# Kernel tuning notes

Measured on AMD Instinct MI355X. Metric: run time of the kernel, lower is better.

Reference implementation:

```python
import jax, jax.numpy as jnp
import numpy as np

N, E = 3000, 48000
IN_C, HID, OUT_C = 16, 64, 16
K1 = (N + 1) // 2          # ceil(0.5*N) = 1500
K2 = (K1 + 1) // 2         # ceil(0.5*K1) = 750


def _glorot(k, fi, fo):
    return jax.random.normal(k, (fi, fo), jnp.float32) / jnp.sqrt(jnp.float32(fi))


def setup_inputs() -> dict:
    key = jax.random.key(0)
    ks = jax.random.split(key, 10)
    x = jax.random.normal(ks[0], (N, IN_C), jnp.float32)
    edge_index = jax.random.randint(ks[1], (2, E), 0, N, dtype=jnp.int32)
    return {
        "x": x,
        "edge_index": edge_index,
        "W0": _glorot(ks[2], IN_C, HID), "b0": jnp.zeros((HID,), jnp.float32),
        "W1": _glorot(ks[3], HID, HID), "b1": jnp.zeros((HID,), jnp.float32),
        "W2": _glorot(ks[4], HID, HID), "b2": jnp.zeros((HID,), jnp.float32),
        "p1": jax.random.normal(ks[5], (HID,), jnp.float32),
        "p2": jax.random.normal(ks[6], (HID,), jnp.float32),
        "Wu0": _glorot(ks[7], HID, HID), "bu0": jnp.zeros((HID,), jnp.float32),
        "Wu1": _glorot(ks[8], HID, OUT_C), "bu1": jnp.zeros((OUT_C,), jnp.float32),
    }


def _gcn(h, A, W, b):
    # GCNConv(improved=True): add self-loops with weight 2, symmetric gcn_norm
    # with degree taken over the target (column) axis; aggregate at targets.
    n = A.shape[0]
    eye = jnp.eye(n, dtype=A.dtype)
    Ah = A + 2.0 * eye
    deg = Ah.sum(axis=0)                      # in-degree (PyG gcn_norm uses col)
    dinv = jnp.where(deg > 0, jax.lax.rsqrt(deg), 0.0)
    M = dinv[:, None] * Ah * dinv[None, :]    # M[s, t] = norm of edge s->t
    return M.T @ (h @ W) + b                  # out[t] = sum_s M[s,t] * h[s] W


def _augment(A):
    # augment_adj: remove self loops, add self loops (w=1), A <- A @ A, drop diag
    n = A.shape[0]
    eye = jnp.eye(n, dtype=A.dtype)
    A1 = A * (1.0 - eye) + eye
    A2 = A1 @ A1
    return A2 * (1.0 - eye)


def _topk_pool(h, A, p, k):
    # TopKPooling defaults: score = tanh((x . p) / ||p||), multiplier = 1
    score = jnp.tanh((h @ p) / jnp.linalg.norm(p))
    _, perm = jax.lax.top_k(score, k)
    hp = h[perm] * score[perm][:, None]
    Ap = A[perm][:, perm]
    return hp, Ap, perm


def _graph_unet(x, A0, W0, b0, W1, b1, W2, b2, p1, p2, Wu0, bu0, Wu1, bu1):
    act = jnp.tanh
    x = act(_gcn(x, A0, W0, b0))
    res0 = x
    # down level 1
    xp, A1, perm1 = _topk_pool(x, _augment(A0), p1, K1)
    x = act(_gcn(xp, A1, W1, b1))
    res1 = x
    # down level 2 (deepest; not stored as residual)
    xp, A2, perm2 = _topk_pool(x, _augment(A1), p2, K2)
    x = act(_gcn(xp, A2, W2, b2))
    # up to level 1 (sum_res=True)
    up = jnp.zeros_like(res1).at[perm2].set(x)
    x = act(_gcn(res1 + up, A1, Wu0, bu0))
    # up to level 0 (last up conv: no activation)
    up = jnp.zeros_like(res0).at[perm1].set(x)
    return _gcn(res0 + up, A0, Wu1, bu1)


def reference(x, edge_index, W0, b0, W1, b1, W2, b2, p1, p2, Wu0, bu0, Wu1, bu1):
    # dense adjacency from COO edge list with unit edge weights (duplicates sum)
    A0 = jnp.zeros((N, N), jnp.float32).at[edge_index[0], edge_index[1]].add(1.0)
    # eval-mode forward of PUnetStepV2: drift = GraphUNet(x, edge_index)
    return _graph_unet(x, A0, W0, b0, W1, b1, W2, b2, p1, p2, Wu0, bu0, Wu1, bu1)
```

## Files before the change

### kernel.cpp

```cpp
#include <hip/hip_runtime.h>

#define NN   3000
#define EE   48000
#define KK1  1500
#define KK2  750
#define KK2P 752
#define HIDC 64
#define SLOT 64

#define CAP0  64
#define CAP1  768
#define CAP2  768
#define CAPB0 64
#define CAPMAX 768


__global__ void k_zero_i32(int* __restrict__ p, int n) {
    int i = blockIdx.x * blockDim.x + threadIdx.x;
    if (i < n) p[i] = 0;
}

__global__ void k_edge_slots(const int* __restrict__ ei, int* __restrict__ cntraw,
                             int* __restrict__ slots) {
    int e = blockIdx.x * blockDim.x + threadIdx.x;
    if (e >= EE) return;
    int s = ei[e];
    int t = ei[EE + e];
    int idx = atomicAdd(&cntraw[t], 1);
    if (idx < SLOT) slots[t * SLOT + idx] = s;
}

__global__ void k_csr0_sort(const int* __restrict__ cntraw, const int* __restrict__ slots,
                            int* __restrict__ cols, float* __restrict__ vals,
                            int* __restrict__ cnt, float* __restrict__ dinv) {
    int row = blockIdx.x * (blockDim.x >> 6) + (threadIdx.x >> 6);
    int lane = threadIdx.x & 63;
    int raw = cntraw[row];
    int nz = raw < SLOT ? raw : SLOT;
    int my = (lane < nz) ? slots[row * SLOT + lane] : 0x7FFFFFFF;
    int dup_before = 0, equal_total = 0;
    for (int f = 0; f < 64; ++f) {
        int cf = __shfl(my, f, 64);
        if (cf == my) { equal_total++; if (f < lane) dup_before++; }
    }
    bool leader = (lane < nz) && (dup_before == 0);
    unsigned long long lm = __ballot(leader);
    int dl = 0;
    unsigned long long m = lm;
    while (m) {
        int f = __builtin_ctzll(m); m &= m - 1;
        int cf = __shfl(my, f, 64);
        dl += (cf < my);
    }
    if (leader) {
        cols[(size_t)row * CAP0 + dl] = my;
        vals[(size_t)row * CAP0 + dl] = (float)equal_total;
    }
    if (lane == 0) {
        cnt[row] = __popcll(lm);
        dinv[row] = rsqrtf((float)raw + 2.0f);
    }
}

__global__ void k_xw_scale(const float* __restrict__ h, const float* __restrict__ up,
                           const int* __restrict__ selpos,
                           const float* __restrict__ W, const float* __restrict__ dinv,
                           float* __restrict__ g, int n, int IC, int OC) {
    int row = blockIdx.x;
    int c = threadIdx.x;
    __shared__ float hr[64];
    if (c < IC) {
        float v = h[(size_t)row * IC + c];
        if (selpos) {
            int sp = selpos[row];
            if (sp >= 0) v += up[(size_t)sp * IC + c];
        }
        hr[c] = v;
    }
    __syncthreads();
    if (c >= OC) return;
    float acc = 0.0f;
    for (int k = 0; k < IC; ++k) acc += hr[k] * W[k * OC + c];
    g[(size_t)row * OC + c] = dinv[row] * acc;
}

__global__ void k_gcn_agg_csr(const int* __restrict__ cols, const float* __restrict__ vals,
                              const int* __restrict__ cnt, int CAP,
                              const float* __restrict__ g, const float* __restrict__ dinv,
                              const float* __restrict__ bias, float* __restrict__ out,
                              int n, int C, int do_tanh,
                              const float* __restrict__ p, float* __restrict__ score) {
    int row = blockIdx.x;
    int w = threadIdx.x >> 6;
    int lane = threadIdx.x & 63;
    int nz = cnt[row];
    const int*   rc = cols + (size_t)row * CAP;
    const float* rv = vals + (size_t)row * CAP;
    bool act = lane < C;
    float a0 = 0.f, a1 = 0.f, a2 = 0.f, a3 = 0.f;
    float a4 = 0.f, a5 = 0.f, a6 = 0.f, a7 = 0.f;
    for (int e = 8 * w; e + 8 <= nz; e += 32) {
        int   c0 = rc[e],     c1 = rc[e + 1], c2 = rc[e + 2], c3 = rc[e + 3];
        int   c4 = rc[e + 4], c5 = rc[e + 5], c6 = rc[e + 6], c7 = rc[e + 7];
        float v0 = rv[e],     v1 = rv[e + 1], v2 = rv[e + 2], v3 = rv[e + 3];
        float v4 = rv[e + 4], v5 = rv[e + 5], v6 = rv[e + 6], v7 = rv[e + 7];
        if (act) {
            a0 += v0 * g[(size_t)c0 * C + lane];
            a1 += v1 * g[(size_t)c1 * C + lane];
            a2 += v2 * g[(size_t)c2 * C + lane];
            a3 += v3 * g[(size_t)c3 * C + lane];
            a4 += v4 * g[(size_t)c4 * C + lane];
            a5 += v5 * g[(size_t)c5 * C + lane];
            a6 += v6 * g[(size_t)c6 * C + lane];
            a7 += v7 * g[(size_t)c7 * C + lane];
        }
    }
    if (w == 0) {
        for (int e = nz & ~7; e < nz; ++e)
            if (act) a0 += rv[e] * g[(size_t)rc[e] * C + lane];
    }
    __shared__ float red[4][64];
    red[w][lane] = ((a0 + a1) + (a2 + a3)) + ((a4 + a5) + (a6 + a7));
    __syncthreads();
    if (w == 0) {
        float o = 0.f;
        if (act) {
            float a = (red[0][lane] + red[1][lane]) + (red[2][lane] + red[3][lane])
                    + 2.0f * g[(size_t)row * C + lane];
            o = dinv[row] * a + bias[lane];
            if (do_tanh) o = tanhf(o);
            out[(size_t)row * C + lane] = o;
        }
        if (p) {
            float pv = p[lane];
            float d = o * pv, pp = pv * pv;
            for (int off = 32; off; off >>= 1) {
                d  += __shfl_down(d, off, 64);
                pp += __shfl_down(pp, off, 64);
            }
            if (lane == 0) score[row] = tanhf(d * rsqrtf(pp));
        }
    }
}

__global__ void k_topk(const float* __restrict__ score, const float* __restrict__ h,
                       int n, int k, int* __restrict__ perm, int* __restrict__ selpos,
                       float* __restrict__ hp) {
    int i = blockIdx.x;
    float si = score[i];
    int r = 0;
    for (int j = threadIdx.x; j < n; j += blockDim.x) {
        float sj = score[j];
        r += (sj > si) || (sj == si && j < i);
    }
    int lane = threadIdx.x & 63, wid = threadIdx.x >> 6;
    for (int off = 32; off; off >>= 1) r += __shfl_down(r, off, 64);
    __shared__ int red[4];
    __shared__ int srank;
    if (lane == 0) red[wid] = r;
    __syncthreads();
    if (threadIdx.x == 0) {
        int rank = red[0] + red[1] + red[2] + red[3];
        srank = rank;
        selpos[i] = (rank < k) ? rank : -1;
        if (rank < k) perm[rank] = i;
    }
    __syncthreads();
    int rank = srank;
    if (rank < k && threadIdx.x < HIDC)
        hp[(size_t)rank * HIDC + threadIdx.x] = h[(size_t)i * HIDC + threadIdx.x] * si;
}

__global__ void k_bcolcsr(const int* __restrict__ cols, const float* __restrict__ vals,
                          const int* __restrict__ cnt, int CAPS,
                          const int* __restrict__ selpos, int n,
                          int* __restrict__ bcC, float* __restrict__ bcV,
                          int* __restrict__ bcN, int CAPB) {
    int row = blockIdx.x * (blockDim.x >> 6) + (threadIdx.x >> 6);
    int lane = threadIdx.x & 63;
    if (row >= n) return;
    int nz = cnt[row];
    int base = 0;
    for (int e0 = 0; e0 < nz; e0 += 64) {
        int e = e0 + lane;
        int j = -1; float v = 0.0f;
        if (e < nz) {
            int c = cols[(size_t)row * CAPS + e];
            if (c != row) { j = selpos[c]; v = vals[(size_t)row * CAPS + e]; }
        }
        unsigned long long mb = __ballot(j >= 0);
        if (j >= 0) {
            int idx = base + __popcll(mb & ((1ull << lane) - 1ull));
            if (idx < CAPB) { bcC[(size_t)row * CAPB + idx] = j; bcV[(size_t)row * CAPB + idx] = v; }
        }
        base += __popcll(mb);
    }
    if (lane == 0) {
        int jd = selpos[row];
        if (jd >= 0 && base < CAPB) {
            bcC[(size_t)row * CAPB + base] = jd;
            bcV[(size_t)row * CAPB + base] = 1.0f;
            base++;
        }
        bcN[row] = base < CAPB ? base : CAPB;
    }
}

__global__ void k_aug_sparse(const int* __restrict__ perm,
                             const int* __restrict__ colsS, const float* __restrict__ valsS,
                             const int* __restrict__ cntS, int CAPS,
                             const int* __restrict__ bcC, const float* __restrict__ bcV,
                             const int* __restrict__ bcN, int CAPB, int kk,
                             int* __restrict__ colsD, float* __restrict__ valsD,
                             int* __restrict__ cntD, float* __restrict__ dinvD, int CAPD) {
    __shared__ float srow[1504];
    __shared__ float ssum[4];
    int i = blockIdx.x;
    int pi = perm[i];
    int nzS = cntS[pi];
    for (int t = threadIdx.x; t < 1504; t += blockDim.x) srow[t] = 0.0f;
    __syncthreads();
    int w = threadIdx.x >> 6, lane = threadIdx.x & 63;
    for (int ee = w; ee <= nzS; ee += 4) {
        int k; float kv;
        if (ee == nzS) { k = pi; kv = 1.0f; }
        else {
            k = colsS[(size_t)pi * CAPS + ee];
            if (k == pi) continue;
            kv = valsS[(size_t)pi * CAPS + ee];
        }
        int bn = bcN[k];
        const int*   bc = bcC + (size_t)k * CAPB;
        const float* bv = bcV + (size_t)k * CAPB;
        for (int t = lane; t < bn; t += 64)
            atomicAdd(&srow[bc[t]], kv * bv[t]);
    }
    __syncthreads();
    if (threadIdx.x == 0) srow[i] = 0.0f;
    __syncthreads();
    float psum = 0.0f;
    for (int t = threadIdx.x; t < kk; t += blockDim.x) psum += srow[t];
    for (int off = 32; off; off >>= 1) psum += __shfl_down(psum, off, 64);
    if (lane == 0) ssum[w] = psum;
    __syncthreads();
    if (w == 0) {
        if (lane == 0)
            dinvD[i] = rsqrtf((ssum[0] + ssum[1]) + (ssum[2] + ssum[3]) + 2.0f);
        int base = 0;
        for (int c0 = 0; c0 < kk; c0 += 64) {
            int c = c0 + lane;
            float v = (c < kk) ? srow[c] : 0.0f;
            unsigned long long mb = __ballot(v != 0.0f);
            if (v != 0.0f) {
                int idx = base + __popcll(mb & ((1ull << lane) - 1ull));
                if (idx < CAPD) {
                    colsD[(size_t)i * CAPD + idx] = c;
                    valsD[(size_t)i * CAPD + idx] = v;
                }
            }
            base += __popcll(mb);
        }
        if (lane == 0) cntD[i] = base < CAPD ? base : CAPD;
    }
}

__global__ void k_bcol_scatter(const int* __restrict__ cols, const float* __restrict__ vals,
                               const int* __restrict__ cnt, int CAP,
                               const int* __restrict__ selpos, float* __restrict__ Bcol, int ldb) {
    int row = blockIdx.x;
    float4* rowp = (float4*)(Bcol + (size_t)row * ldb);
    float4 z = {0.f, 0.f, 0.f, 0.f};
    for (int q = threadIdx.x; q < (ldb >> 2); q += blockDim.x) rowp[q] = z;
    __syncthreads();
    int nz = cnt[row];
    for (int e = threadIdx.x; e < nz; e += blockDim.x) {
        int c = cols[(size_t)row * CAP + e];
        if (c == row) continue;
        int j = selpos[c];
        if (j >= 0) Bcol[(size_t)row * ldb + j] = vals[(size_t)row * CAP + e];
    }
    if (threadIdx.x == 0) {
        int j = selpos[row];
        if (j >= 0) Bcol[(size_t)row * ldb + j] = 1.0f;
    }
}

__global__ void k_aug_fused(const int* __restrict__ perm,
                            const int* __restrict__ colsS, const float* __restrict__ valsS,
                            const int* __restrict__ cntS, int CAPS,
                            const float* __restrict__ Bcol, int ldb, int kk,
                            int* __restrict__ colsD, float* __restrict__ valsD,
                            int* __restrict__ cntD, float* __restrict__ dinvD, int CAPD) {
    __shared__ int   scol[CAPMAX];
    __shared__ float sval[CAPMAX];
    __shared__ float srow[1504];
    __shared__ float ssum[4];
    int i = blockIdx.x;
    int pi = perm[i];
    int nz = cntS[pi];
    for (int e = threadIdx.x; e < nz; e += blockDim.x) {
        int c = colsS[(size_t)pi * CAPS + e];
        scol[e] = c;
        sval[e] = (c == pi) ? 0.0f : valsS[(size_t)pi * CAPS + e];
    }
    __syncthreads();
    float psum = 0.0f;
    for (int j0 = threadIdx.x * 4; j0 < kk; j0 += blockDim.x * 4) {
        int j4 = j0 >> 2;
        float4 a = ((const float4*)(Bcol + (size_t)pi * ldb))[j4];
        float4 acc1 = {0.f, 0.f, 0.f, 0.f};
        int e = 0;
        for (; e + 8 <= nz; e += 8) {
            float v0 = sval[e],     v1 = sval[e + 1], v2 = sval[e + 2], v3 = sval[e + 3];
            float v4 = sval[e + 4], v5 = sval[e + 5], v6 = sval[e + 6], v7 = sval[e + 7];
            float4 b0 = ((const float4*)(Bcol + (size_t)scol[e]     * ldb))[j4];
            float4 b1 = ((const float4*)(Bcol + (size_t)scol[e + 1] * ldb))[j4];
            float4 b2 = ((const float4*)(Bcol + (size_t)scol[e + 2] * ldb))[j4];
            float4 b3 = ((const float4*)(Bcol + (size_t)scol[e + 3] * ldb))[j4];
            float4 b4 = ((const float4*)(Bcol + (size_t)scol[e + 4] * ldb))[j4];
            float4 b5 = ((const float4*)(Bcol + (size_t)scol[e + 5] * ldb))[j4];
            float4 b6 = ((const float4*)(Bcol + (size_t)scol[e + 6] * ldb))[j4];
            float4 b7 = ((const float4*)(Bcol + (size_t)scol[e + 7] * ldb))[j4];
            a.x += v0 * b0.x + v1 * b1.x + v2 * b2.x + v3 * b3.x;
            a.y += v0 * b0.y + v1 * b1.y + v2 * b2.y + v3 * b3.y;
            a.z += v0 * b0.z + v1 * b1.z + v2 * b2.z + v3 * b3.z;
            a.w += v0 * b0.w + v1 * b1.w + v2 * b2.w + v3 * b3.w;
            acc1.x += v4 * b4.x + v5 * b5.x + v6 * b6.x + v7 * b7.x;
            acc1.y += v4 * b4.y + v5 * b5.y + v6 * b6.y + v7 * b7.y;
            acc1.z += v4 * b4.z + v5 * b5.z + v6 * b6.z + v7 * b7.z;
            acc1.w += v4 * b4.w + v5 * b5.w + v6 * b6.w + v7 * b7.w;
        }
        for (; e < nz; ++e) {
            float v = sval[e];
            float4 b = ((const float4*)(Bcol + (size_t)scol[e] * ldb))[j4];
            a.x += v * b.x; a.y += v * b.y; a.z += v * b.z; a.w += v * b.w;
        }
        a.x += acc1.x; a.y += acc1.y; a.z += acc1.z; a.w += acc1.w;
        if (i >= j0 && i < j0 + 4) ((float*)&a)[i - j0] = 0.0f;
        *(float4*)(srow + j0) = a;
        psum += (a.x + a.y) + (a.z + a.w);
    }
    int lane = threadIdx.x & 63, w = threadIdx.x >> 6;
    for (int off = 32; off; off >>= 1) psum += __shfl_down(psum, off, 64);
    if (lane == 0) ssum[w] = psum;
    __syncthreads();
    if (w == 0) {
        if (lane == 0)
            dinvD[i] = rsqrtf((ssum[0] + ssum[1]) + (ssum[2] + ssum[3]) + 2.0f);
        int base = 0;
        for (int c0 = 0; c0 < kk; c0 += 64) {
            int c = c0 + lane;
            float v = (c < kk) ? srow[c] : 0.0f;
            unsigned long long mb = __ballot(v != 0.0f);
            if (v != 0.0f) {
                int idx = base + __popcll(mb & ((1ull << lane) - 1ull));
                if (idx < CAPD) {
                    colsD[(size_t)i * CAPD + idx] = c;
                    valsD[(size_t)i * CAPD + idx] = v;
                }
            }
            base += __popcll(mb);
        }
        if (lane == 0) cntD[i] = base < CAPD ? base : CAPD;
    }
}


extern "C" void kernel_launch(void* const* d_in, const int* in_sizes, int n_in,
                              void* d_out, int out_size, void* d_ws, size_t ws_size,
                              hipStream_t stream) {
    const float* x   = (const float*)d_in[0];
    const int*   ei  = (const int*)d_in[1];
    const float* W0  = (const float*)d_in[2];
    const float* b0  = (const float*)d_in[3];
    const float* W1  = (const float*)d_in[4];
    const float* b1  = (const float*)d_in[5];
    const float* W2  = (const float*)d_in[6];
    const float* b2  = (const float*)d_in[7];
    const float* p1  = (const float*)d_in[8];
    const float* p2  = (const float*)d_in[9];
    const float* Wu0 = (const float*)d_in[10];
    const float* bu0 = (const float*)d_in[11];
    const float* Wu1 = (const float*)d_in[12];
    const float* bu1 = (const float*)d_in[13];
    float* out = (float*)d_out;

    float* fw = (float*)d_ws;
    size_t off = 0;
    int*   slots  = (int*)(fw + off); off += (size_t)NN * SLOT;
    int*   cntraw = (int*)(fw + off); off += NN;
    int*   cols0  = (int*)(fw + off); off += (size_t)NN * CAP0;
    float* vals0  = fw + off;         off += (size_t)NN * CAP0;
    int*   cols1  = (int*)(fw + off); off += (size_t)KK1 * CAP1;
    float* vals1  = fw + off;         off += (size_t)KK1 * CAP1;
    int*   cols2  = (int*)(fw + off); off += (size_t)KK2 * CAP2;
    float* vals2  = fw + off;         off += (size_t)KK2 * CAP2;
    int*   bc0C   = (int*)(fw + off); off += (size_t)NN * CAPB0;
    float* bc0V   = fw + off;         off += (size_t)NN * CAPB0;
    int*   bc0N   = (int*)(fw + off); off += NN;
    float* Bcol2  = fw + off;         off += (size_t)KK1 * KK2P;
    int*   cnt0   = (int*)(fw + off); off += NN;
    int*   cnt1   = (int*)(fw + off); off += KK1;
    int*   cnt2   = (int*)(fw + off); off += KK2 + 2;
    float* g      = fw + off; off += (size_t)NN * HIDC;
    float* res0   = fw + off; off += (size_t)NN * HIDC;
    float* res1   = fw + off; off += (size_t)KK1 * HIDC;
    float* hp     = fw + off; off += (size_t)KK1 * HIDC;
    float* hp2    = fw + off; off += (size_t)KK2 * HIDC;
    float* x2     = fw + off; off += (size_t)KK2 * HIDC;
    float* xu     = fw + off; off += (size_t)KK1 * HIDC;
    float* sc1    = fw + off; off += NN;
    float* sc2    = fw + off; off += KK1;
    float* dinv0  = fw + off; off += NN;
    float* dinv1  = fw + off; off += KK1;
    float* dinv2  = fw + off; off += KK2 + 2;
    int* perm1    = (int*)(fw + off); off += KK1;
    int* perm2    = (int*)(fw + off); off += KK2 + 2;
    int* selpos1  = (int*)(fw + off); off += NN;
    int* selpos2  = (int*)(fw + off); off += KK1;
    if (ws_size < off * sizeof(float)) return;

    dim3 b64(64), b256(256);

    k_zero_i32<<<dim3((NN + 255) / 256), b256, 0, stream>>>(cntraw, NN);
    k_edge_slots<<<dim3((EE + 255) / 256), b256, 0, stream>>>(ei, cntraw, slots);
    k_csr0_sort<<<dim3(NN / 4), b256, 0, stream>>>(cntraw, slots, cols0, vals0, cnt0, dinv0);

    k_xw_scale<<<dim3(NN), b64, 0, stream>>>(x, nullptr, nullptr, W0, dinv0, g, NN, 16, 64);
    k_gcn_agg_csr<<<dim3(NN), b256, 0, stream>>>(cols0, vals0, cnt0, CAP0, g, dinv0, b0, res0, NN, 64, 1, p1, sc1);

    k_topk<<<dim3(NN), b256, 0, stream>>>(sc1, res0, NN, KK1, perm1, selpos1, hp);
    k_bcolcsr<<<dim3(NN / 4), b256, 0, stream>>>(cols0, vals0, cnt0, CAP0, selpos1, NN, bc0C, bc0V, bc0N, CAPB0);
    k_aug_sparse<<<dim3(KK1), b256, 0, stream>>>(perm1, cols0, vals0, cnt0, CAP0,
                                                 bc0C, bc0V, bc0N, CAPB0, KK1,
                                                 cols1, vals1, cnt1, dinv1, CAP1);

    k_xw_scale<<<dim3(KK1), b64, 0, stream>>>(hp, nullptr, nullptr, W1, dinv1, g, KK1, 64, 64);
    k_gcn_agg_csr<<<dim3(KK1), b256, 0, stream>>>(cols1, vals1, cnt1, CAP1, g, dinv1, b1, res1, KK1, 64, 1, p2, sc2);

    k_topk<<<dim3(KK1), b256, 0, stream>>>(sc2, res1, KK1, KK2, perm2, selpos2, hp2);
    k_bcol_scatter<<<dim3(KK1), b256, 0, stream>>>(cols1, vals1, cnt1, CAP1, selpos2, Bcol2, KK2P);
    k_aug_fused<<<dim3(KK2), b256, 0, stream>>>(perm2, cols1, vals1, cnt1, CAP1,
                                                Bcol2, KK2P, KK2, cols2, vals2, cnt2, dinv2, CAP2);

    k_xw_scale<<<dim3(KK2), b64, 0, stream>>>(hp2, nullptr, nullptr, W2, dinv2, g, KK2, 64, 64);
    k_gcn_agg_csr<<<dim3(KK2), b256, 0, stream>>>(cols2, vals2, cnt2, CAP2, g, dinv2, b2, x2, KK2, 64, 1, nullptr, nullptr);

    k_xw_scale<<<dim3(KK1), b64, 0, stream>>>(res1, x2, selpos2, Wu0, dinv1, g, KK1, 64, 64);
    k_gcn_agg_csr<<<dim3(KK1), b256, 0, stream>>>(cols1, vals1, cnt1, CAP1, g, dinv1, bu0, xu, KK1, 64, 1, nullptr, nullptr);

    k_xw_scale<<<dim3(NN), b64, 0, stream>>>(res0, xu, selpos1, Wu1, dinv0, g, NN, 64, 16);
    k_gcn_agg_csr<<<dim3(NN), b256, 0, stream>>>(cols0, vals0, cnt0, CAP0, g, dinv0, bu1, out, NN, 16, 0, nullptr, nullptr);
}
```

Before: 161.7 us.

## Split level-2 augment SpGEMM across nonzero chunks with separate CSR build pass

Replaces the fused per-row augment kernel with a split-K version: each output row is computed by four blocks that each handle a quarter of the source row's nonzeros and write partial dense rows to a workspace buffer. A new kernel then sums the four partials, drops the diagonal, compacts the nonzeros into CSR and computes the degree normalisation. This raises parallelism from 750 blocks to 3000 smaller blocks for the latency-bound gather loop. In exchange it adds an extra launch and writes and rereads about 9 MB of partial rows.

Result: faster. 153.2 us (-5.3%).

```diff
diff --git a/kernel.cpp b/kernel.cpp
--- a/kernel.cpp
+++ b/kernel.cpp
@@ -7,6 +7,7 @@
 #define KK2P 752
 #define HIDC 64
 #define SLOT 64
+#define ESPLIT 4
 
 #define CAP0  64
 #define CAP1  768
@@ -285,17 +286,14 @@
     }
 }
 
-__global__ void k_aug_fused(const int* __restrict__ perm,
-                            const int* __restrict__ colsS, const float* __restrict__ valsS,
-                            const int* __restrict__ cntS, int CAPS,
-                            const float* __restrict__ Bcol, int ldb, int kk,
-                            int* __restrict__ colsD, float* __restrict__ valsD,
-                            int* __restrict__ cntD, float* __restrict__ dinvD, int CAPD) {
+__global__ void k_aug_part(const int* __restrict__ perm,
+                           const int* __restrict__ colsS, const float* __restrict__ valsS,
+                           const int* __restrict__ cntS, int CAPS,
+                           const float* __restrict__ Bcol, int ldb, int kk,
+                           float* __restrict__ T2p) {
     __shared__ int   scol[CAPMAX];
     __shared__ float sval[CAPMAX];
-    __shared__ float srow[1504];
-    __shared__ float ssum[4];
-    int i = blockIdx.x;
+    int i = blockIdx.x, sp = blockIdx.y;
     int pi = perm[i];
     int nz = cntS[pi];
     for (int e = threadIdx.x; e < nz; e += blockDim.x) {
@@ -304,64 +302,74 @@
         sval[e] = (c == pi) ? 0.0f : valsS[(size_t)pi * CAPS + e];
     }
     __syncthreads();
-    float psum = 0.0f;
-    for (int j0 = threadIdx.x * 4; j0 < kk; j0 += blockDim.x * 4) {
-        int j4 = j0 >> 2;
-        float4 a = ((const float4*)(Bcol + (size_t)pi * ldb))[j4];
-        float4 acc1 = {0.f, 0.f, 0.f, 0.f};
-        int e = 0;
-        for (; e + 8 <= nz; e += 8) {
-            float v0 = sval[e],     v1 = sval[e + 1], v2 = sval[e + 2], v3 = sval[e + 3];
-            float v4 = sval[e + 4], v5 = sval[e + 5], v6 = sval[e + 6], v7 = sval[e + 7];
-            float4 b0 = ((const float4*)(Bcol + (size_t)scol[e]     * ldb))[j4];
-            float4 b1 = ((const float4*)(Bcol + (size_t)scol[e + 1] * ldb))[j4];
-            float4 b2 = ((const float4*)(Bcol + (size_t)scol[e + 2] * ldb))[j4];
-            float4 b3 = ((const float4*)(Bcol + (size_t)scol[e + 3] * ldb))[j4];
-            float4 b4 = ((const float4*)(Bcol + (size_t)scol[e + 4] * ldb))[j4];
-            float4 b5 = ((const float4*)(Bcol + (size_t)scol[e + 5] * ldb))[j4];
-            float4 b6 = ((const float4*)(Bcol + (size_t)scol[e + 6] * ldb))[j4];
-            float4 b7 = ((const float4*)(Bcol + (size_t)scol[e + 7] * ldb))[j4];
-            a.x += v0 * b0.x + v1 * b1.x + v2 * b2.x + v3 * b3.x;
-            a.y += v0 * b0.y + v1 * b1.y + v2 * b2.y + v3 * b3.y;
-            a.z += v0 * b0.z + v1 * b1.z + v2 * b2.z + v3 * b3.z;
-            a.w += v0 * b0.w + v1 * b1.w + v2 * b2.w + v3 * b3.w;
-            acc1.x += v4 * b4.x + v5 * b5.x + v6 * b6.x + v7 * b7.x;
-            acc1.y += v4 * b4.y + v5 * b5.y + v6 * b6.y + v7 * b7.y;
-            acc1.z += v4 * b4.z + v5 * b5.z + v6 * b6.z + v7 * b7.z;
-            acc1.w += v4 * b4.w + v5 * b5.w + v6 * b6.w + v7 * b7.w;
-        }
-        for (; e < nz; ++e) {
-            float v = sval[e];
-            float4 b = ((const float4*)(Bcol + (size_t)scol[e] * ldb))[j4];
-            a.x += v * b.x; a.y += v * b.y; a.z += v * b.z; a.w += v * b.w;
-        }
-        a.x += acc1.x; a.y += acc1.y; a.z += acc1.z; a.w += acc1.w;
-        if (i >= j0 && i < j0 + 4) ((float*)&a)[i - j0] = 0.0f;
-        *(float4*)(srow + j0) = a;
-        psum += (a.x + a.y) + (a.z + a.w);
-    }
-    int lane = threadIdx.x & 63, w = threadIdx.x >> 6;
-    for (int off = 32; off; off >>= 1) psum += __shfl_down(psum, off, 64);
-    if (lane == 0) ssum[w] = psum;
-    __syncthreads();
-    if (w == 0) {
-        if (lane == 0)
-            dinvD[i] = rsqrtf((ssum[0] + ssum[1]) + (ssum[2] + ssum[3]) + 2.0f);
-        int base = 0;
-        for (int c0 = 0; c0 < kk; c0 += 64) {
-            int c = c0 + lane;
-            float v = (c < kk) ? srow[c] : 0.0f;
-            unsigned long long mb = __ballot(v != 0.0f);
-            if (v != 0.0f) {
-                int idx = base + __popcll(mb & ((1ull << lane) - 1ull));
-                if (idx < CAPD) {
-                    colsD[(size_t)i * CAPD + idx] = c;
-                    valsD[(size_t)i * CAPD + idx] = v;
-                }
+    int j0 = threadIdx.x * 4;
+    if (j0 >= ldb) return;
+    int j4 = j0 >> 2;
+    float4 a = {0.f, 0.f, 0.f, 0.f};
+    if (sp == 0) a = ((const float4*)(Bcol + (size_t)pi * ldb))[j4];
+    float4 acc1 = {0.f, 0.f, 0.f, 0.f};
+    int e  = (nz * sp) / ESPLIT;
+    int e1 = (nz * (sp + 1)) / ESPLIT;
+    for (; e + 8 <= e1; e += 8) {
+        float v0 = sval[e],     v1 = sval[e + 1], v2 = sval[e + 2], v3 = sval[e + 3];
+        float v4 = sval[e + 4], v5 = sval[e + 5], v6 = sval[e + 6], v7 = sval[e + 7];
+        float4 b0 = ((const float4*)(Bcol + (size_t)scol[e]     * ldb))[j4];
+        float4 b1 = ((const float4*)(Bcol + (size_t)scol[e + 1] * ldb))[j4];
+        float4 b2 = ((const float4*)(Bcol + (size_t)scol[e + 2] * ldb))[j4];
+        float4 b3 = ((const float4*)(Bcol + (size_t)scol[e + 3] * ldb))[j4];
+        float4 b4 = ((const float4*)(Bcol + (size_t)scol[e + 4] * ldb))[j4];
+        float4 b5 = ((const float4*)(Bcol + (size_t)scol[e + 5] * ldb))[j4];
+        float4 b6 = ((const float4*)(Bcol + (size_t)scol[e + 6] * ldb))[j4];
+        float4 b7 = ((const float4*)(Bcol + (size_t)scol[e + 7] * ldb))[j4];
+        a.x += v0 * b0.x + v1 * b1.x + v2 * b2.x + v3 * b3.x;
+        a.y += v0 * b0.y + v1 * b1.y + v2 * b2.y + v3 * b3.y;
+        a.z += v0 * b0.z + v1 * b1.z + v2 * b2.z + v3 * b3.z;
+        a.w += v0 * b0.w + v1 * b1.w + v2 * b2.w + v3 * b3.w;
+        acc1.x += v4 * b4.x + v5 * b5.x + v6 * b6.x + v7 * b7.x;
+        acc1.y += v4 * b4.y + v5 * b5.y + v6 * b6.y + v7 * b7.y;
+        acc1.z += v4 * b4.z + v5 * b5.z + v6 * b6.z + v7 * b7.z;
+        acc1.w += v4 * b4.w + v5 * b5.w + v6 * b6.w + v7 * b7.w;
+    }
+    for (; e < e1; ++e) {
+        float v = sval[e];
+        float4 b = ((const float4*)(Bcol + (size_t)scol[e] * ldb))[j4];
+        a.x += v * b.x; a.y += v * b.y; a.z += v * b.z; a.w += v * b.w;
+    }
+    a.x += acc1.x; a.y += acc1.y; a.z += acc1.z; a.w += acc1.w;
+    *(float4*)(T2p + ((size_t)sp * KK2 + i) * ldb + j0) = a;
+}
+
+__global__ void k_csr2_build(const float* __restrict__ T2p,
+                             int* __restrict__ cols, float* __restrict__ vals,
+                             int* __restrict__ cnt, float* __restrict__ dinv) {
+    int row = blockIdx.x * (blockDim.x >> 6) + (threadIdx.x >> 6);
+    int lane = threadIdx.x & 63;
+    if (row >= KK2) return;
+    const float* r0 = T2p + ((size_t)0 * KK2 + row) * KK2P;
+    const float* r1 = T2p + ((size_t)1 * KK2 + row) * KK2P;
+    const float* r2 = T2p + ((size_t)2 * KK2 + row) * KK2P;
+    const float* r3 = T2p + ((size_t)3 * KK2 + row) * KK2P;
+    int base = 0;
+    float s = 0.0f;
+    for (int c0 = 0; c0 < KK2; c0 += 64) {
+        int c = c0 + lane;
+        float v = 0.0f;
+        if (c < KK2 && c != row) v = (r0[c] + r1[c]) + (r2[c] + r3[c]);
+        unsigned long long mb = __ballot(v != 0.0f);
+        if (v != 0.0f) {
+            int idx = base + __popcll(mb & ((1ull << lane) - 1ull));
+            if (idx < CAP2) {
+                cols[(size_t)row * CAP2 + idx] = c;
+                vals[(size_t)row * CAP2 + idx] = v;
             }
-            base += __popcll(mb);
-        }
-        if (lane == 0) cntD[i] = base < CAPD ? base : CAPD;
+            s += v;
+        }
+        base += __popcll(mb);
+    }
+    for (int off = 32; off; off >>= 1) s += __shfl_down(s, off, 64);
+    if (lane == 0) {
+        cnt[row] = base < CAP2 ? base : CAP2;
+        dinv[row] = rsqrtf(s + 2.0f);
     }
 }
 
@@ -399,6 +407,7 @@
     float* bc0V   = fw + off;         off += (size_t)NN * CAPB0;
     int*   bc0N   = (int*)(fw + off); off += NN;
     float* Bcol2  = fw + off;         off += (size_t)KK1 * KK2P;
+    float* T2p    = fw + off;         off += (size_t)ESPLIT * KK2 * KK2P;
     int*   cnt0   = (int*)(fw + off); off += NN;
     int*   cnt1   = (int*)(fw + off); off += KK1;
     int*   cnt2   = (int*)(fw + off); off += KK2 + 2;
@@ -420,7 +429,7 @@
     int* selpos2  = (int*)(fw + off); off += KK1;
     if (ws_size < off * sizeof(float)) return;
 
-    dim3 b64(64), b256(256);
+    dim3 b64(64), b192(192), b256(256);
 
     k_zero_i32<<<dim3((NN + 255) / 256), b256, 0, stream>>>(cntraw, NN);
     k_edge_slots<<<dim3((EE + 255) / 256), b256, 0, stream>>>(ei, cntraw, slots);
@@ -440,8 +449,9 @@
 
     k_topk<<<dim3(KK1), b256, 0, stream>>>(sc2, res1, KK1, KK2, perm2, selpos2, hp2);
     k_bcol_scatter<<<dim3(KK1), b256, 0, stream>>>(cols1, vals1, cnt1, CAP1, selpos2, Bcol2, KK2P);
-    k_aug_fused<<<dim3(KK2), b256, 0, stream>>>(perm2, cols1, vals1, cnt1, CAP1,
-                                                Bcol2, KK2P, KK2, cols2, vals2, cnt2, dinv2, CAP2);
+    k_aug_part<<<dim3(KK2, ESPLIT), b192, 0, stream>>>(perm2, cols1, vals1, cnt1, CAP1,
+                                                       Bcol2, KK2P, KK2, T2p);
+    k_csr2_build<<<dim3((KK2 + 3) / 4), b256, 0, stream>>>(T2p, cols2, vals2, cnt2, dinv2);
 
     k_xw_scale<<<dim3(KK2), b64, 0, stream>>>(hp2, nullptr, nullptr, W2, dinv2, g, KK2, 64, 64);
     k_gcn_agg_csr<<<dim3(KK2), b256, 0, stream>>>(cols2, vals2, cnt2, CAP2, g, dinv2, b2, x2, KK2, 64, 1, nullptr, nullptr);
```
